# Performance work log

Measured on AMD Instinct MI355X. Metric: run time of the kernel, lower is better.

Reference implementation:

```python
import jax, jax.numpy as jnp
import numpy as np

B, N, D = 32768, 50, 128  # batch, neighbours, embedding_dim


def setup_inputs() -> dict:
    key = jax.random.key(0)
    k1, k2, k3, k4 = jax.random.split(key, 4)
    scale = 1.0 / np.sqrt(D)
    return {
        "mainNodeEmbed": jax.random.normal(k1, (B, D), dtype=jnp.float32),
        "neighbourNodesEmbeds": jax.random.normal(k2, (B, N, D), dtype=jnp.float32),
        "W": jax.random.normal(k3, (D, D), dtype=jnp.float32) * scale,            # self.w kernel (no bias)
        "A_w": jax.random.normal(k4, (2 * D, D), dtype=jnp.float32) * scale,      # attentionDense kernel
        "A_b": jnp.zeros((D,), dtype=jnp.float32),                                 # attentionDense bias
    }


def reference(mainNodeEmbed, neighbourNodesEmbeds, W, A_w, A_b):
    # Linear projections (shared weight, no bias)
    px = mainNodeEmbed @ W                       # [B, D]
    pn = neighbourNodesEmbeds @ W                # [B, N, D]
    # mode == 'repeat': tile main node across neighbours, concat on feature dim
    px_rep = jnp.broadcast_to(px[:, None, :], pn.shape)   # [B, N, D]
    cat = jnp.concatenate([px_rep, pn], axis=2)           # [B, N, 2D]
    # attention logits: Dense + leaky_relu (tf default alpha=0.2)
    e_ij = jax.nn.leaky_relu(cat @ A_w + A_b, negative_slope=0.2)  # [B, N, D]
    # softmax over the neighbour axis (axis=1), per feature channel
    a_ij = jax.nn.softmax(e_ij, axis=1)
    # attention-weighted sum over neighbours
    return jnp.sum(a_ij * pn, axis=1)            # [B, D]
```

## Files before the change

kernel.cpp:

```cpp
#include <hip/hip_runtime.h>
#include <math.h>

#define NN 50
#define DD 128
#define MT 4
#define KT 4
#define NIT 64
#define TILE_H 12800

typedef __attribute__((ext_vector_type(4))) float  f32x4;
typedef __attribute__((ext_vector_type(2))) __fp16 f16x2;
typedef __attribute__((ext_vector_type(4))) __fp16 f16x4;
typedef __attribute__((ext_vector_type(8))) __fp16 f16x8;

__device__ float g_WA1f[DD * DD];
__device__ float g_WA2f[DD * DD];
__device__ __attribute__((aligned(16))) __fp16 g_Wt[2 * DD * DD];
__device__ __attribute__((aligned(16))) __fp16 g_W1t[DD * DD];

__global__ void compute_WA(const float* __restrict__ W,
                           const float* __restrict__ A_w) {
    const int d = threadIdx.x, k = blockIdx.x, m = blockIdx.y;
    const float* __restrict__ A = A_w + (size_t)m * DD * DD;
    float acc = 0.f;
#pragma unroll 8
    for (int j = 0; j < DD; ++j)
        acc = fmaf(W[k * DD + j], A[j * DD + d], acc);
    if (m == 0) g_WA1f[k * DD + d] = acc;
    else        g_WA2f[k * DD + d] = acc;
}

__global__ void cvt_weights(const float* __restrict__ W) {
    const int n = blockIdx.x;
    const int k = threadIdx.x;
    if (n < DD)          g_Wt[n * DD + k]             = (__fp16)W[k * DD + n];
    else if (n < 2 * DD) g_Wt[n * DD + k]             = (__fp16)g_WA2f[k * DD + (n - DD)];
    else                 g_W1t[(n - 2 * DD) * DD + k] = (__fp16)g_WA1f[k * DD + (n - 2 * DD)];
}

__device__ __forceinline__ f16x8 cvt8(float4 f0, float4 f1) {
    union { f16x2 h[4]; f16x8 v; } u;
    u.h[0] = __builtin_amdgcn_cvt_pkrtz(f0.x, f0.y);
    u.h[1] = __builtin_amdgcn_cvt_pkrtz(f0.z, f0.w);
    u.h[2] = __builtin_amdgcn_cvt_pkrtz(f1.x, f1.y);
    u.h[3] = __builtin_amdgcn_cvt_pkrtz(f1.z, f1.w);
    return u.v;
}

#define MFMA(a, b, c) __builtin_amdgcn_mfma_f32_16x16x32_f16((a), (b), (c), 0, 0, 0)

__global__ __launch_bounds__(512, 4)
void attn_mfma(const float* __restrict__ x,
               const float* __restrict__ nbr,
               const float* __restrict__ A_b,
               float* __restrict__ out, int B) {
    __shared__ __attribute__((aligned(16))) char tiles[2][TILE_H];
    __shared__ float pxa_lds[NIT][DD];

    const int tid  = threadIdx.x;
    const int w    = tid >> 6;
    const int lane = tid & 63;
    const int c    = lane & 15;
    const int g    = lane >> 4;
    const size_t b0 = (size_t)blockIdx.x * NIT;
    const int col  = 16 * w + c;

    {
        f32x4 pacc[MT];
#pragma unroll
        for (int mt = 0; mt < MT; ++mt) pacc[mt] = (f32x4)0.f;
#pragma unroll
        for (int mt = 0; mt < MT; ++mt) {
            long brow = (long)b0 + 16 * mt + c;
            if (brow > B - 1) brow = B - 1;
            const float4* __restrict__ xp =
                reinterpret_cast<const float4*>(x + brow * DD);
#pragma unroll
            for (int kt = 0; kt < KT; ++kt) {
                const f16x8 a = cvt8(xp[8 * kt + 2 * g], xp[8 * kt + 2 * g + 1]);
                const f16x8 bw = *reinterpret_cast<const f16x8*>(
                    g_W1t + col * DD + 32 * kt + 8 * g);
                pacc[mt] = MFMA(a, bw, pacc[mt]);
            }
        }
        const float ab = A_b[col];
#pragma unroll
        for (int mt = 0; mt < MT; ++mt)
#pragma unroll
            for (int r = 0; r < 4; ++r)
                pxa_lds[16 * mt + 4 * g + r][col] = pacc[mt][r] + ab;
    }

    f16x8 bF[2][KT];
#pragma unroll
    for (int p = 0; p < 2; ++p)
#pragma unroll
        for (int kt = 0; kt < KT; ++kt) {
            bF[p][kt] = *reinterpret_cast<const f16x8*>(
                g_Wt + (p * DD + col) * DD + 32 * kt + 8 * g);
            asm volatile("" : "+v"(bF[p][kt]));
        }

    f32x4 ra[4];

    auto nb4_of = [&](int it) {
        int itc = it < NIT ? it : NIT - 1;
        size_t bidx = b0 + (size_t)itc;
        if (bidx > (size_t)(B - 1)) bidx = (size_t)(B - 1);
        return reinterpret_cast<const f32x4*>(nbr + bidx * (size_t)(NN * DD));
    };
    auto load_half = [&](int it, int hf) {
        const f32x4* __restrict__ nb4 = nb4_of(it);
#pragma unroll
        for (int j = 2 * hf; j < 2 * hf + 2; ++j) {
            const int p = w + 8 * j;
            if (p < 25)
                ra[j] = __builtin_nontemporal_load(nb4 + p * 64 + lane);
        }
    };

    auto write_tile = [&](char* dst) {
#pragma unroll
        for (int j = 0; j < 4; ++j) {
            const int p = w + 8 * j;
            if (p < 25) {
                const int lb  = p * 512 + lane * 8;
                const int row = lb >> 8;
                const int ad  = lb ^ ((row & 7) << 4);
                union { f16x2 h[2]; f16x4 v; } u;
                u.h[0] = __builtin_amdgcn_cvt_pkrtz(ra[j][0], ra[j][1]);
                u.h[1] = __builtin_amdgcn_cvt_pkrtz(ra[j][2], ra[j][3]);
                *reinterpret_cast<f16x4*>(dst + ad) = u.v;
            }
        }
    };

    auto compute_half = [&](const char* tile, f32x4 (&acc)[MT][2], int mt0) {
#pragma unroll
        for (int mt = mt0; mt < mt0 + 2; ++mt) {
            int row = 16 * mt + c;
            if (row > NN - 1) row = NN - 1;
            const int rb = row * 256;
            const int sw = (row & 7) << 4;
#pragma unroll
            for (int kt = 0; kt < KT; ++kt) {
                const f16x8 a = *reinterpret_cast<const f16x8*>(
                    tile + ((rb + kt * 64 + g * 16) ^ sw));
                acc[mt][0] = MFMA(a, bF[0][kt], acc[mt][0]);
                acc[mt][1] = MFMA(a, bF[1][kt], acc[mt][1]);
            }
        }
    };

    load_half(0, 0); load_half(0, 1);
    write_tile(tiles[0]);
    load_half(1, 0); load_half(1, 1);
    asm volatile("s_waitcnt lgkmcnt(0)" ::: "memory");
    __builtin_amdgcn_sched_barrier(0);
    __builtin_amdgcn_s_barrier();

    const float m0v = (g == 0) ? 1.f : 0.f;

#pragma unroll 1
    for (int i = 0; i < NIT; ++i) {
        write_tile(tiles[(i + 1) & 1]);
        load_half(i + 2, 0);
        __builtin_amdgcn_sched_barrier(0);

        const char* __restrict__ tile = tiles[i & 1];
        f32x4 acc[MT][2];
#pragma unroll
        for (int mt = 0; mt < MT; ++mt)
#pragma unroll
            for (int p = 0; p < 2; ++p) acc[mt][p] = (f32x4)0.f;

        compute_half(tile, acc, 0);

        load_half(i + 2, 1);
        __builtin_amdgcn_sched_barrier(0);

        compute_half(tile, acc, 2);

        {
            const float pxa = pxa_lds[i][col];
            float den = 0.f, num = 0.f;
#pragma unroll
            for (int mt = 0; mt < MT; ++mt)
#pragma unroll
                for (int r = 0; r < 4; ++r) {
                    if (mt == 3 && r >= 2) continue;
                    float t = pxa + acc[mt][1][r];
                    t = fmaxf(t, 0.2f * t);
                    float p = __expf(t);
                    if (mt == 3) p *= m0v;
                    den += p;
                    num = fmaf(p, acc[mt][0][r], num);
                }
            den += __shfl_xor(den, 16); den += __shfl_xor(den, 32);
            num += __shfl_xor(num, 16); num += __shfl_xor(num, 32);
            if (g == 0 && b0 + i < (size_t)B)
                out[(b0 + i) * DD + col] = __fdividef(num, den);
        }

        asm volatile("s_waitcnt lgkmcnt(0)" ::: "memory");
        __builtin_amdgcn_sched_barrier(0);
        __builtin_amdgcn_s_barrier();
    }
}

extern "C" void kernel_launch(void* const* d_in, const int* in_sizes, int n_in,
                              void* d_out, int out_size, void* d_ws, size_t ws_size,
                              hipStream_t stream) {
    const float* x   = (const float*)d_in[0];
    const float* nbr = (const float*)d_in[1];
    const float* W   = (const float*)d_in[2];
    const float* A_w = (const float*)d_in[3];
    const float* A_b = (const float*)d_in[4];
    float* out = (float*)d_out;
    const int B = in_sizes[0] / DD;

    compute_WA<<<dim3(DD, 2), DD, 0, stream>>>(W, A_w);
    cvt_weights<<<3 * DD, DD, 0, stream>>>(W);
    const int grid = (B + NIT - 1) / NIT;
    attn_mfma<<<grid, 512, 0, stream>>>(x, nbr, A_b, out, B);
}
```

Before: 212.0 us.

## Split neighbour rows across wave groups and exchange partial softmax sums via LDS

```diff
diff --git a/kernel.cpp b/kernel.cpp
--- a/kernel.cpp
+++ b/kernel.cpp
@@ -3,7 +3,6 @@
 
 #define NN 50
 #define DD 128
-#define MT 4
 #define KT 4
 #define NIT 64
 #define TILE_H 12800
@@ -56,21 +55,24 @@
                float* __restrict__ out, int B) {
     __shared__ __attribute__((aligned(16))) char tiles[2][TILE_H];
     __shared__ float pxa_lds[NIT][DD];
+    __shared__ float exch[2][4][2][2][16];
 
     const int tid  = threadIdx.x;
     const int w    = tid >> 6;
     const int lane = tid & 63;
     const int c    = lane & 15;
     const int g    = lane >> 4;
+    const int rg   = w >> 2;
+    const int cg   = w & 3;
     const size_t b0 = (size_t)blockIdx.x * NIT;
-    const int col  = 16 * w + c;
 
     {
-        f32x4 pacc[MT];
-#pragma unroll
-        for (int mt = 0; mt < MT; ++mt) pacc[mt] = (f32x4)0.f;
-#pragma unroll
-        for (int mt = 0; mt < MT; ++mt) {
+        const int pcol = 16 * w + c;
+        f32x4 pacc[4];
+#pragma unroll
+        for (int mt = 0; mt < 4; ++mt) pacc[mt] = (f32x4)0.f;
+#pragma unroll
+        for (int mt = 0; mt < 4; ++mt) {
             long brow = (long)b0 + 16 * mt + c;
             if (brow > B - 1) brow = B - 1;
             const float4* __restrict__ xp =
@@ -79,27 +81,30 @@
             for (int kt = 0; kt < KT; ++kt) {
                 const f16x8 a = cvt8(xp[8 * kt + 2 * g], xp[8 * kt + 2 * g + 1]);
                 const f16x8 bw = *reinterpret_cast<const f16x8*>(
-                    g_W1t + col * DD + 32 * kt + 8 * g);
+                    g_W1t + pcol * DD + 32 * kt + 8 * g);
                 pacc[mt] = MFMA(a, bw, pacc[mt]);
             }
         }
-        const float ab = A_b[col];
-#pragma unroll
-        for (int mt = 0; mt < MT; ++mt)
+        const float ab = A_b[pcol];
+#pragma unroll
+        for (int mt = 0; mt < 4; ++mt)
 #pragma unroll
             for (int r = 0; r < 4; ++r)
-                pxa_lds[16 * mt + 4 * g + r][col] = pacc[mt][r] + ab;
+                pxa_lds[16 * mt + 4 * g + r][pcol] = pacc[mt][r] + ab;
     }
 
-    f16x8 bF[2][KT];
+    f16x8 bF[2][2][KT];
 #pragma unroll
     for (int p = 0; p < 2; ++p)
 #pragma unroll
-        for (int kt = 0; kt < KT; ++kt) {
-            bF[p][kt] = *reinterpret_cast<const f16x8*>(
-                g_Wt + (p * DD + col) * DD + 32 * kt + 8 * g);
-            asm volatile("" : "+v"(bF[p][kt]));
-        }
+        for (int nt = 0; nt < 2; ++nt)
+#pragma unroll
+            for (int kt = 0; kt < KT; ++kt) {
+                const int colx = p * DD + 32 * cg + 16 * nt + c;
+                bF[p][nt][kt] = *reinterpret_cast<const f16x8*>(
+                    g_Wt + colx * DD + 32 * kt + 8 * g);
+                asm volatile("" : "+v"(bF[p][nt][kt]));
+            }
 
     f32x4 ra[4];
 
@@ -135,20 +140,20 @@
         }
     };
 
-    auto compute_half = [&](const char* tile, f32x4 (&acc)[MT][2], int mt0) {
-#pragma unroll
-        for (int mt = mt0; mt < mt0 + 2; ++mt) {
-            int row = 16 * mt + c;
-            if (row > NN - 1) row = NN - 1;
-            const int rb = row * 256;
-            const int sw = (row & 7) << 4;
-#pragma unroll
-            for (int kt = 0; kt < KT; ++kt) {
-                const f16x8 a = *reinterpret_cast<const f16x8*>(
-                    tile + ((rb + kt * 64 + g * 16) ^ sw));
-                acc[mt][0] = MFMA(a, bF[0][kt], acc[mt][0]);
-                acc[mt][1] = MFMA(a, bF[1][kt], acc[mt][1]);
-            }
+    auto compute_mt = [&](const char* tile, f32x4 (&acc)[2][2][2], int mt) {
+        int row = 16 * (2 * rg + mt) + c;
+        if (row > NN - 1) row = NN - 1;
+        const int rb = row * 256;
+        const int sw = (row & 7) << 4;
+#pragma unroll
+        for (int kt = 0; kt < KT; ++kt) {
+            const f16x8 a = *reinterpret_cast<const f16x8*>(
+                tile + ((rb + kt * 64 + g * 16) ^ sw));
+#pragma unroll
+            for (int p = 0; p < 2; ++p)
+#pragma unroll
+                for (int nt = 0; nt < 2; ++nt)
+                    acc[mt][p][nt] = MFMA(a, bF[p][nt][kt], acc[mt][p][nt]);
         }
     };
 
@@ -168,43 +173,63 @@
         __builtin_amdgcn_sched_barrier(0);
 
         const char* __restrict__ tile = tiles[i & 1];
-        f32x4 acc[MT][2];
-#pragma unroll
-        for (int mt = 0; mt < MT; ++mt)
-#pragma unroll
-            for (int p = 0; p < 2; ++p) acc[mt][p] = (f32x4)0.f;
-
-        compute_half(tile, acc, 0);
+        f32x4 acc[2][2][2];
+#pragma unroll
+        for (int mt = 0; mt < 2; ++mt)
+#pragma unroll
+            for (int p = 0; p < 2; ++p)
+#pragma unroll
+                for (int nt = 0; nt < 2; ++nt) acc[mt][p][nt] = (f32x4)0.f;
+
+        compute_mt(tile, acc, 0);
 
         load_half(i + 2, 1);
         __builtin_amdgcn_sched_barrier(0);
 
-        compute_half(tile, acc, 2);
-
-        {
-            const float pxa = pxa_lds[i][col];
-            float den = 0.f, num = 0.f;
-#pragma unroll
-            for (int mt = 0; mt < MT; ++mt)
+        compute_mt(tile, acc, 1);
+
+        float num[2], den[2];
+#pragma unroll
+        for (int nt = 0; nt < 2; ++nt) {
+            const float pxa = pxa_lds[i][32 * cg + 16 * nt + c];
+            float d_ = 0.f, n_ = 0.f;
+#pragma unroll
+            for (int mt = 0; mt < 2; ++mt)
 #pragma unroll
                 for (int r = 0; r < 4; ++r) {
-                    if (mt == 3 && r >= 2) continue;
-                    float t = pxa + acc[mt][1][r];
+                    if (rg == 1 && mt == 1 && r >= 2) continue;
+                    float t = pxa + acc[mt][1][nt][r];
                     t = fmaxf(t, 0.2f * t);
-                    float p = __expf(t);
-                    if (mt == 3) p *= m0v;
-                    den += p;
-                    num = fmaf(p, acc[mt][0][r], num);
+                    float e = __expf(t);
+                    if (rg == 1 && mt == 1) e *= m0v;
+                    d_ += e;
+                    n_ = fmaf(e, acc[mt][0][nt][r], n_);
                 }
-            den += __shfl_xor(den, 16); den += __shfl_xor(den, 32);
-            num += __shfl_xor(num, 16); num += __shfl_xor(num, 32);
-            if (g == 0 && b0 + i < (size_t)B)
-                out[(b0 + i) * DD + col] = __fdividef(num, den);
+            d_ += __shfl_xor(d_, 16); d_ += __shfl_xor(d_, 32);
+            n_ += __shfl_xor(n_, 16); n_ += __shfl_xor(n_, 32);
+            num[nt] = n_; den[nt] = d_;
+        }
+        if (rg == 1 && g == 0) {
+#pragma unroll
+            for (int nt = 0; nt < 2; ++nt) {
+                exch[i & 1][cg][nt][0][c] = num[nt];
+                exch[i & 1][cg][nt][1][c] = den[nt];
+            }
         }
 
         asm volatile("s_waitcnt lgkmcnt(0)" ::: "memory");
         __builtin_amdgcn_sched_barrier(0);
         __builtin_amdgcn_s_barrier();
+
+        if (rg == 0 && g == 0) {
+#pragma unroll
+            for (int nt = 0; nt < 2; ++nt) {
+                const float nT = num[nt] + exch[i & 1][cg][nt][0][c];
+                const float dT = den[nt] + exch[i & 1][cg][nt][1][c];
+                __builtin_nontemporal_store(__fdividef(nT, dT),
+                    out + (b0 + i) * DD + 32 * cg + 16 * nt + c);
+            }
+        }
     }
 }
 
```

Result: slower. 471.7 us (+122.5%).
